# Kernel optimization log

Hardware: AMD Instinct MI355X
Metric: run time of the kernel (lower is better)

Reference implementation:

```python
import jax, jax.numpy as jnp
import numpy as np

EMBED = 192
EXPAND = 3
D1 = EMBED * EXPAND  # 576
RPE_IN = 32
LAYERS = 3
LAMBDA = 0.95


def _rpe_mlp(t, w0, b0, ws, bs, wo, bo):
    # t: (2n, 1) relative positions -> (2n, D1) Toeplitz coefficients
    h = t @ w0.T + b0
    for i in range(ws.shape[0]):
        h = jax.nn.relu(h) @ ws[i].T + bs[i]
    return jax.nn.relu(h) @ wo.T + bo


def _toeplitz(x, a):
    # Toeplitz matmul via length-2n circular convolution (FFT).
    # x: (B, n, d); a: (2n, d) coeffs ordered [t0, t1..t_{n-1}, pad, neg half]
    n = x.shape[1]
    m = 2 * n
    xf = jnp.fft.rfft(x, m, axis=1)
    af = jnp.fft.rfft(a, m, axis=0)
    return jnp.fft.irfft(xf * af[None], m, axis=1)[:, :n]


def _forward(x, p_w, p_b, q_w, q_b, v_w, v_b, o_w, o_b, slope,
             t1_w0, t1_b0, t1_ws, t1_bs, t1_wo, t1_bo,
             t2_w0, t2_b0, t2_ws, t2_bs, t2_wo, t2_bo):
    b, h, w, d = x.shape
    n = h  # square grid: h == w, rpe/decay built from n = x.shape[1]
    dt = x.dtype

    pos = jnp.arange(1, n, dtype=dt).reshape(-1, 1)          # (n-1, 1)
    zero = jnp.zeros((1, 1), dt)
    rpe_input = jnp.concatenate([zero, pos, zero, -pos], axis=0)  # (2n, 1)

    p = jax.nn.silu(x @ p_w.T + p_b)
    q = jax.nn.silu(x @ q_w.T + q_b)
    v = jax.nn.silu(x @ v_w.T + v_b)

    # decay mask: slope clamped to [0,1], blended with lambda, powered by |lag|
    sl = LAMBDA + (1.0 - LAMBDA) * jnp.clip(slope, 0.0, 1.0)  # (1, D1)
    idx = jnp.arange(1, n, dtype=dt).reshape(1, -1, 1)        # (1, n-1, 1)
    gamma = sl ** idx                                          # (1, n-1, D1)
    one = jnp.ones((1, 1, D1), dt)
    decay = jnp.concatenate([one, gamma, one, gamma[:, ::-1]], axis=1)[0]  # (2n, D1)

    a1 = _rpe_mlp(rpe_input, t1_w0, t1_b0, t1_ws, t1_bs, t1_wo, t1_bo) * decay
    a2 = _rpe_mlp(rpe_input, t2_w0, t2_b0, t2_ws, t2_bs, t2_wo, t2_bo) * decay

    qv = q * v                                                 # (b, h, w, D1)
    # axial mixing: tno1 along width, tno2 along height
    o1 = _toeplitz(qv.reshape(b * h, w, D1), a1).reshape(b, h, w, D1)
    o2 = _toeplitz(jnp.transpose(qv, (0, 2, 1, 3)).reshape(b * w, h, D1), a2)
    o2 = jnp.transpose(o2.reshape(b, w, h, D1), (0, 2, 1, 3))
    out = p * (o1 + o2)
    return out @ o_w.T + o_b


def setup_inputs() -> dict:
    key = jax.random.key(0)
    ks = jax.random.split(key, 8)

    def lin(k, out_d, in_d):
        k1, k2 = jax.random.split(k)
        s = 1.0 / np.sqrt(in_d)
        return (jax.random.uniform(k1, (out_d, in_d), jnp.float32, -s, s),
                jax.random.uniform(k2, (out_d,), jnp.float32, -s, s))

    x = jax.random.normal(ks[0], (8, 56, 56, EMBED), jnp.float32)
    p_w, p_b = lin(ks[1], D1, EMBED)
    q_w, q_b = lin(ks[2], D1, EMBED)
    v_w, v_b = lin(ks[3], D1, EMBED)
    o_w, o_b = lin(ks[4], EMBED, D1)
    # slope init: 1/arange(1, d1+1)^(1/(index+1)), index=0
    slope = (1.0 / jnp.arange(1, D1 + 1, dtype=jnp.float32)).reshape(1, -1)

    def tno_params(kb):
        kk = jax.random.split(kb, 2 + LAYERS)
        w0, b0 = lin(kk[0], RPE_IN, 1)
        ws, bs = [], []
        for i in range(LAYERS):
            wi, bi = lin(kk[1 + i], RPE_IN, RPE_IN)
            ws.append(wi); bs.append(bi)
        wo, bo = lin(kk[1 + LAYERS], D1, RPE_IN)
        return w0, b0, jnp.stack(ws), jnp.stack(bs), wo, bo

    t1 = tno_params(ks[5])
    t2 = tno_params(ks[6])
    return {"x": x, "p_w": p_w, "p_b": p_b, "q_w": q_w, "q_b": q_b,
            "v_w": v_w, "v_b": v_b, "o_w": o_w, "o_b": o_b, "slope": slope,
            "t1_w0": t1[0], "t1_b0": t1[1], "t1_ws": t1[2], "t1_bs": t1[3], "t1_wo": t1[4], "t1_bo": t1[5],
            "t2_w0": t2[0], "t2_b0": t2[1], "t2_ws": t2[2], "t2_bs": t2[3], "t2_wo": t2[4], "t2_bo": t2[5]}


def reference(x, p_w, p_b, q_w, q_b, v_w, v_b, o_w, o_b, slope,
              t1_w0, t1_b0, t1_ws, t1_bs, t1_wo, t1_bo,
              t2_w0, t2_b0, t2_ws, t2_bs, t2_wo, t2_bo):
    return _forward(x, p_w, p_b, q_w, q_b, v_w, v_b, o_w, o_b, slope,
                    t1_w0, t1_b0, t1_ws, t1_bs, t1_wo, t1_bo,
                    t2_w0, t2_b0, t2_ws, t2_bs, t2_wo, t2_bo)
```

## Files before the change

### kernel.cpp

```cpp
#include <hip/hip_runtime.h>
#include <hip/hip_bf16.h>
#include <math.h>

typedef unsigned short u16;
typedef short bf16x8 __attribute__((ext_vector_type(8)));
typedef float f32x4 __attribute__((ext_vector_type(4)));

#define NB 8
#define NN 56
#define M2 112
#define EMB 192
#define D1 576
#define TOK (NB*NN*NN)

__device__ __forceinline__ float bf2f(unsigned int u) {
    union { unsigned int i; float f; } v; v.i = u << 16; return v.f;
}
__device__ __forceinline__ u16 f2bf(float f) {
    union { float f; unsigned int i; } v; v.f = f;
    unsigned int x = v.i;
    return (u16)((x + 0x7fffu + ((x >> 16) & 1u)) >> 16);
}
__device__ __forceinline__ float silu(float x) {
    return x / (1.0f + __expf(-x));
}
__device__ __forceinline__ void async16(void* lds, const void* g) {
    __builtin_amdgcn_global_load_lds(
        (const __attribute__((address_space(1))) void*)g,
        (__attribute__((address_space(3))) void*)lds, 16, 0, 0);
}

#define XCH (TOK*EMB/4)
#define WCH (D1*EMB/4)
__global__ __launch_bounds__(256) void convert_kernel(
    const float* __restrict__ x,
    const float* __restrict__ pw, const float* __restrict__ qw,
    const float* __restrict__ vw, const float* __restrict__ ow,
    u16* __restrict__ xb, u16* __restrict__ wb, u16* __restrict__ owb)
{
    int tid = blockIdx.x * 256 + threadIdx.x;
    const float* src; u16* dst; int off;
    if (tid < XCH) { src = x; dst = xb; off = tid; }
    else {
        int r = tid - XCH;
        int seg = r / WCH; off = r % WCH;
        if (seg == 0)      { src = pw; dst = wb; }
        else if (seg == 1) { src = qw; dst = wb + D1*EMB; }
        else if (seg == 2) { src = vw; dst = wb + 2*D1*EMB; }
        else if (seg == 3) { src = ow; dst = owb; }
        else return;
    }
    float4 f = *(const float4*)(src + off * 4);
    ushort4 o;
    o.x = f2bf(f.x); o.y = f2bf(f.y); o.z = f2bf(f.z); o.w = f2bf(f.w);
    *(ushort4*)(dst + off * 4) = o;
}

__global__ __launch_bounds__(576) void rpe_kernel(
    const float* __restrict__ slope,
    const float* w0a, const float* b0a, const float* wsa, const float* bsa,
    const float* woa, const float* boa,
    const float* w0b, const float* b0b, const float* wsb, const float* bsb,
    const float* wob, const float* bob,
    float* __restrict__ A1, float* __restrict__ A2)
{
    int wq  = blockIdx.x / M2;
    int row = blockIdx.x % M2;
    const float* w0 = wq ? w0b : w0a;  const float* b0 = wq ? b0b : b0a;
    const float* ws = wq ? wsb : wsa;  const float* bs = wq ? bsb : bsa;
    const float* wo = wq ? wob : woa;  const float* bo = wq ? bob : boa;
    float* A = wq ? A2 : A1;

    float tval = (row == 0 || row == 56) ? 0.0f
               : (row < 56 ? (float)row : -(float)(row - 56));
    int kexp = (row == 0 || row == 56) ? 0 : (row < 56 ? row : 112 - row);

    __shared__ float h[32], g[32];
    int t = threadIdx.x;
    if (t < 32) h[t] = tval * w0[t] + b0[t];
    __syncthreads();
    for (int L = 0; L < 3; L++) {
        if (t < 32) g[t] = fmaxf(h[t], 0.0f);
        __syncthreads();
        float hn = 0.0f;
        if (t < 32) {
            hn = bs[L * 32 + t];
            for (int k = 0; k < 32; k++)
                hn = fmaf(g[k], ws[(L * 32 + t) * 32 + k], hn);
        }
        __syncthreads();
        if (t < 32) h[t] = hn;
        __syncthreads();
    }
    if (t < 32) g[t] = fmaxf(h[t], 0.0f);
    __syncthreads();

    float o = bo[t];
    for (int k = 0; k < 32; k++)
        o = fmaf(g[k], wo[t * 32 + k], o);

    float sl = slope[t];
    sl = 0.95f + 0.05f * fminf(fmaxf(sl, 0.0f), 1.0f);
    float dec = powf(sl, (float)kexp);
    A[row * D1 + t] = o * dec;
}

__global__ __launch_bounds__(256) void tbuild_kernel(
    const float* __restrict__ A1, const float* __restrict__ A2,
    u16* __restrict__ T1t, u16* __restrict__ T2t)
{
    int d = blockIdx.x;
    const float* src = blockIdx.y ? A2 : A1;
    u16* dst = blockIdx.y ? T2t : T1t;
    __shared__ float win[111];
    int t = threadIdx.x;
    if (t < 111) {
        int lag = t - 55;
        int rowi = lag + (lag < 0 ? 112 : 0);
        win[t] = src[rowi * D1 + d];
    }
    __syncthreads();
    int i = t >> 2, jq = (t & 3) * 16;
    u16 vals[16];
    #pragma unroll
    for (int jj = 0; jj < 16; jj++) {
        int j = jq + jj;
        float v = (i < 56 && j < 56) ? win[i - j + 55] : 0.0f;
        vals[jj] = f2bf(v);
    }
    u16* out = dst + ((size_t)d * 64 + i) * 64 + jq;
    *(uint4*)(out)     = *(uint4*)&vals[0];
    *(uint4*)(out + 8) = *(uint4*)&vals[8];
}

__global__ __launch_bounds__(256) void proj_kernel(
    const u16* __restrict__ xb, const u16* __restrict__ wb,
    const float* __restrict__ pb, const float* __restrict__ qb,
    const float* __restrict__ vb,
    u16* __restrict__ P_T, u16* __restrict__ QV_T)
{
    __shared__ u16 lds[40960];
    int m0 = blockIdx.x * 128, n0 = blockIdx.y * 64;
    int t = threadIdx.x;
    int l = t & 63, wave = t >> 6;
    int wm = wave >> 1, wn = wave & 1;
    int col16 = l & 15, q = l >> 4;

    f32x4 accp[4][2], accq[4][2], accv[4][2];
    #pragma unroll
    for (int i = 0; i < 4; i++)
        #pragma unroll
        for (int j = 0; j < 2; j++) {
            accp[i][j] = (f32x4){0,0,0,0};
            accq[i][j] = (f32x4){0,0,0,0};
            accv[i][j] = (f32x4){0,0,0,0};
        }

    auto stage = [&](int kc, int buf) {
        int bo = buf * 20480;
        #pragma unroll
        for (int ii = 0; ii < 4; ii++) {
            int slot = (ii * 4 + wave) * 64 + l;
            int r = slot >> 3, s = slot & 7;
            int g = s ^ (r & 7);
            async16(&lds[bo + slot * 8], xb + (m0 + r) * EMB + kc * 64 + g * 8);
        }
        #pragma unroll
        for (int ii = 0; ii < 6; ii++) {
            int slot = (ii * 4 + wave) * 64 + l;
            int mat = slot >> 9, cc = slot & 511;
            int r = cc >> 3, s = cc & 7;
            int g = s ^ (r & 7);
            async16(&lds[bo + 8192 + slot * 8],
                    wb + mat * (D1 * EMB) + (n0 + r) * EMB + kc * 64 + g * 8);
        }
    };

    stage(0, 0);
    __syncthreads();

    #pragma unroll
    for (int kc = 0; kc < 3; kc++) {
        int buf = kc & 1;
        if (kc < 2) stage(kc + 1, buf ^ 1);
        int bo = buf * 20480;
        #pragma unroll
        for (int kk = 0; kk < 2; kk++) {
            bf16x8 af[4];
            #pragma unroll
            for (int mt = 0; mt < 4; mt++) {
                int row = wm * 64 + mt * 16 + col16;
                int sw = (q + 4 * kk) ^ (col16 & 7);
                af[mt] = *(const bf16x8*)&lds[bo + row * 64 + sw * 8];
            }
            bf16x8 bfr[3][2];
            #pragma unroll
            for (int mat = 0; mat < 3; mat++)
                #pragma unroll
                for (int nt = 0; nt < 2; nt++) {
                    int row = wn * 32 + nt * 16 + col16;
                    int sw = (q + 4 * kk) ^ (col16 & 7);
                    bfr[mat][nt] = *(const bf16x8*)&lds[bo + 8192 + mat * 4096 + row * 64 + sw * 8];
                }
            #pragma unroll
            for (int mt = 0; mt < 4; mt++)
                #pragma unroll
                for (int nt = 0; nt < 2; nt++) {
                    accp[mt][nt] = __builtin_amdgcn_mfma_f32_16x16x32_bf16(
                        af[mt], bfr[0][nt], accp[mt][nt], 0, 0, 0);
                    accq[mt][nt] = __builtin_amdgcn_mfma_f32_16x16x32_bf16(
                        af[mt], bfr[1][nt], accq[mt][nt], 0, 0, 0);
                    accv[mt][nt] = __builtin_amdgcn_mfma_f32_16x16x32_bf16(
                        af[mt], bfr[2][nt], accv[mt][nt], 0, 0, 0);
                }
        }
        __syncthreads();
    }

    u16* scr = lds + wave * 2688;
    float pbv[2], qbv[2], vbv[2];
    #pragma unroll
    for (int nt = 0; nt < 2; nt++) {
        int n = n0 + wn * 32 + nt * 16 + col16;
        pbv[nt] = pb[n]; qbv[nt] = qb[n]; vbv[nt] = vb[n];
    }
    int tok = (l & 31) * 2;
    int dh = l >> 5;
    #pragma unroll
    for (int mt = 0; mt < 4; mt++)
        #pragma unroll
        for (int nt = 0; nt < 2; nt++)
            #pragma unroll
            for (int r = 0; r < 4; r++)
                scr[(mt * 16 + q * 4 + r) * 42 + nt * 16 + col16] =
                    f2bf(silu(accp[mt][nt][r] + pbv[nt]));
    #pragma unroll
    for (int i = 0; i < 16; i++) {
        int dl = i * 2 + dh;
        unsigned int v = (unsigned int)scr[tok * 42 + dl] |
                         ((unsigned int)scr[(tok + 1) * 42 + dl] << 16);
        *(unsigned int*)&P_T[(size_t)(n0 + wn * 32 + dl) * TOK + m0 + wm * 64 + tok] = v;
    }
    #pragma unroll
    for (int mt = 0; mt < 4; mt++)
        #pragma unroll
        for (int nt = 0; nt < 2; nt++)
            #pragma unroll
            for (int r = 0; r < 4; r++)
                scr[(mt * 16 + q * 4 + r) * 42 + nt * 16 + col16] =
                    f2bf(silu(accq[mt][nt][r] + qbv[nt]) *
                         silu(accv[mt][nt][r] + vbv[nt]));
    #pragma unroll
    for (int i = 0; i < 16; i++) {
        int dl = i * 2 + dh;
        unsigned int v = (unsigned int)scr[tok * 42 + dl] |
                         ((unsigned int)scr[(tok + 1) * 42 + dl] << 16);
        *(unsigned int*)&QV_T[(size_t)(n0 + wn * 32 + dl) * TOK + m0 + wm * 64 + tok] = v;
    }
}

__global__ __launch_bounds__(256) void tno_mfma(
    const u16* __restrict__ QV_T, const u16* __restrict__ T1t,
    const u16* __restrict__ T2t, const u16* __restrict__ P_T,
    u16* __restrict__ U_T)
{
    __shared__ u16 T1s[4096];
    __shared__ u16 T2s[4096];
    __shared__ u16 Qn[64 * 72];
    __shared__ u16 Qt[64 * 72];
    __shared__ float O1f[56 * 68];
    int d = blockIdx.x, b = blockIdx.y;
    int t = threadIdx.x;
    size_t base = (size_t)d * TOK + (size_t)b * 3136;

    #pragma unroll
    for (int k = 0; k < 2; k++) {
        int slot = t + k * 256;
        int i = slot >> 3, s = slot & 7;
        int g = s ^ (i & 7);
        async16(&T1s[slot * 8], T1t + ((size_t)d * 64 + i) * 64 + g * 8);
        async16(&T2s[slot * 8], T2t + ((size_t)d * 64 + i) * 64 + g * 8);
    }
    for (int c = t; c < 392; c += 256) {
        int h = c / 7, w8 = (c % 7) * 8;
        uint4 v = *(const uint4*)(QV_T + base + c * 8);
        *(uint4*)&Qn[h * 72 + w8] = v;
        u16 e[8];
        *(uint4*)e = v;
        #pragma unroll
        for (int k = 0; k < 8; k++)
            Qt[(w8 + k) * 72 + h] = e[k];
    }
    if (t < 56) {
        uint4 z = {0, 0, 0, 0};
        *(uint4*)&Qn[t * 72 + 56] = z;
        *(uint4*)&Qt[t * 72 + 56] = z;
    }
    __syncthreads();

    int l = t & 63, wave = t >> 6;
    int col16 = l & 15, q = l >> 4;

    f32x4 acc1[4], acc2[4];
    #pragma unroll
    for (int i = 0; i < 4; i++) { acc1[i] = (f32x4){0,0,0,0}; acc2[i] = (f32x4){0,0,0,0}; }

    #pragma unroll
    for (int kk = 0; kk < 2; kk++) {
        int sw = ((q + 4 * kk) ^ (col16 & 7)) * 8;
        bf16x8 bq1 = *(const bf16x8*)&Qn[(wave * 16 + col16) * 72 + kk * 32 + q * 8];
        bf16x8 bq2 = *(const bf16x8*)&Qt[(wave * 16 + col16) * 72 + kk * 32 + q * 8];
        #pragma unroll
        for (int mt = 0; mt < 4; mt++) {
            bf16x8 a1 = *(const bf16x8*)&T1s[(mt * 16 + col16) * 64 + sw];
            bf16x8 a2 = *(const bf16x8*)&T2s[(mt * 16 + col16) * 64 + sw];
            acc1[mt] = __builtin_amdgcn_mfma_f32_16x16x32_bf16(a1, bq1, acc1[mt], 0, 0, 0);
            acc2[mt] = __builtin_amdgcn_mfma_f32_16x16x32_bf16(a2, bq2, acc2[mt], 0, 0, 0);
        }
    }

    {
        int n = wave * 16 + col16;
        if (n < 56) {
            #pragma unroll
            for (int mt = 0; mt < 4; mt++)
                #pragma unroll
                for (int r = 0; r < 4; r++) {
                    int m = mt * 16 + q * 4 + r;
                    if (m < 56) O1f[n * 68 + m] = acc1[mt][r];
                }
        }
    }
    __syncthreads();
    {
        int n = wave * 16 + col16;
        if (n < 56) {
            #pragma unroll
            for (int mt = 0; mt < 4; mt++)
                #pragma unroll
                for (int r = 0; r < 4; r++) {
                    int m = mt * 16 + q * 4 + r;
                    if (m < 56) O1f[m * 68 + n] += acc2[mt][r];
                }
        }
    }
    __syncthreads();
    for (int c = t; c < 392; c += 256) {
        int h = c / 7, w8 = (c % 7) * 8;
        f32x4 s0 = *(const f32x4*)&O1f[h * 68 + w8];
        f32x4 s1 = *(const f32x4*)&O1f[h * 68 + w8 + 4];
        uint4 pv = *(const uint4*)(P_T + base + c * 8);
        u16 pe[8];
        *(uint4*)pe = pv;
        u16 ue[8];
        #pragma unroll
        for (int k = 0; k < 4; k++) ue[k] = f2bf(bf2f(pe[k]) * s0[k]);
        #pragma unroll
        for (int k = 0; k < 4; k++) ue[4 + k] = f2bf(bf2f(pe[4 + k]) * s1[k]);
        *(uint4*)(U_T + base + c * 8) = *(uint4*)ue;
    }
}

__global__ __launch_bounds__(256) void transp_kernel(
    const u16* __restrict__ U_T, u16* __restrict__ U)
{
    __shared__ u16 tile[64 * 72];
    int t = threadIdx.x;
    int t0 = blockIdx.x * 64;
    int d0 = blockIdx.y * 64;
    {
        int dr = t >> 2, c = t & 3;
        #pragma unroll
        for (int h = 0; h < 2; h++) {
            int cc = c + h * 4;
            uint4 v = *(const uint4*)(U_T + (size_t)(d0 + dr) * TOK + t0 + cc * 8);
            *(uint4*)&tile[dr * 72 + cc * 8] = v;
        }
    }
    __syncthreads();
    {
        int tr = t & 63, c4 = t >> 6;
        u16 vals[16];
        #pragma unroll
        for (int k = 0; k < 16; k++)
            vals[k] = tile[(c4 * 16 + k) * 72 + tr];
        u16* dst = U + (size_t)(t0 + tr) * D1 + d0 + c4 * 16;
        *(uint4*)(dst)     = *(uint4*)&vals[0];
        *(uint4*)(dst + 8) = *(uint4*)&vals[8];
    }
}

__global__ __launch_bounds__(256) void outproj_kernel(
    const u16* __restrict__ U, const u16* __restrict__ owb,
    const float* __restrict__ ob, float* __restrict__ out)
{
    __shared__ char ldsraw[36864];
    u16* As = (u16*)ldsraw;
    u16* Bs = (u16*)(ldsraw + 16384);
    int m0 = blockIdx.x * 128, n0 = blockIdx.y * 64;
    int t = threadIdx.x;
    int l = t & 63, wave = t >> 6;
    int wm = wave >> 1, wn = wave & 1;
    int col16 = l & 15, q = l >> 4;

    f32x4 acc[4][2];
    #pragma unroll
    for (int i = 0; i < 4; i++)
        #pragma unroll
        for (int j = 0; j < 2; j++) acc[i][j] = (f32x4){0,0,0,0};

    for (int k0 = 0; k0 < D1; k0 += 64) {
        #pragma unroll
        for (int ii = 0; ii < 4; ii++) {
            int slot = (ii * 4 + wave) * 64 + l;
            int r = slot >> 3, s = slot & 7;
            int g = s ^ (r & 7);
            async16(&As[slot * 8], U + (m0 + r) * D1 + k0 + g * 8);
        }
        #pragma unroll
        for (int ii = 0; ii < 2; ii++) {
            int slot = (ii * 4 + wave) * 64 + l;
            int r = slot >> 3, s = slot & 7;
            int g = s ^ (r & 7);
            async16(&Bs[slot * 8], owb + (n0 + r) * D1 + k0 + g * 8);
        }
        __syncthreads();

        #pragma unroll
        for (int kk = 0; kk < 2; kk++) {
            int sw = (q + 4 * kk) ^ (col16 & 7);
            bf16x8 af[4];
            #pragma unroll
            for (int mt = 0; mt < 4; mt++)
                af[mt] = *(const bf16x8*)&As[(wm * 64 + mt * 16 + col16) * 64 + sw * 8];
            bf16x8 bfr[2];
            #pragma unroll
            for (int nt = 0; nt < 2; nt++)
                bfr[nt] = *(const bf16x8*)&Bs[(wn * 32 + nt * 16 + col16) * 64 + sw * 8];
            #pragma unroll
            for (int mt = 0; mt < 4; mt++)
                #pragma unroll
                for (int nt = 0; nt < 2; nt++)
                    acc[mt][nt] = __builtin_amdgcn_mfma_f32_16x16x32_bf16(
                        af[mt], bfr[nt], acc[mt][nt], 0, 0, 0);
        }
        __syncthreads();
    }

    float* scr = (float*)ldsraw + wave * 2304;
    float obv[2];
    #pragma unroll
    for (int nt = 0; nt < 2; nt++)
        obv[nt] = ob[n0 + wn * 32 + nt * 16 + col16];
    #pragma unroll
    for (int mt = 0; mt < 4; mt++)
        #pragma unroll
        for (int nt = 0; nt < 2; nt++)
            #pragma unroll
            for (int r = 0; r < 4; r++)
                scr[(mt * 16 + q * 4 + r) * 36 + nt * 16 + col16] =
                    acc[mt][nt][r] + obv[nt];
    #pragma unroll
    for (int k = 0; k < 8; k++) {
        int row = k * 8 + (l >> 3), cs = (l & 7) * 4;
        f32x4 v = *(const f32x4*)&scr[row * 36 + cs];
        *(f32x4*)&out[(m0 + wm * 64 + row) * EMB + n0 + wn * 32 + cs] = v;
    }
}

extern "C" void kernel_launch(void* const* d_in, const int* in_sizes, int n_in,
                              void* d_out, int out_size, void* d_ws, size_t ws_size,
                              hipStream_t stream)
{
    (void)in_sizes; (void)n_in; (void)out_size; (void)ws_size;
    const float* x     = (const float*)d_in[0];
    const float* p_w   = (const float*)d_in[1];
    const float* p_b   = (const float*)d_in[2];
    const float* q_w   = (const float*)d_in[3];
    const float* q_b   = (const float*)d_in[4];
    const float* v_w   = (const float*)d_in[5];
    const float* v_b   = (const float*)d_in[6];
    const float* o_w   = (const float*)d_in[7];
    const float* o_b   = (const float*)d_in[8];
    const float* slope = (const float*)d_in[9];
    const float* t1_w0 = (const float*)d_in[10];
    const float* t1_b0 = (const float*)d_in[11];
    const float* t1_ws = (const float*)d_in[12];
    const float* t1_bs = (const float*)d_in[13];
    const float* t1_wo = (const float*)d_in[14];
    const float* t1_bo = (const float*)d_in[15];
    const float* t2_w0 = (const float*)d_in[16];
    const float* t2_b0 = (const float*)d_in[17];
    const float* t2_ws = (const float*)d_in[18];
    const float* t2_bs = (const float*)d_in[19];
    const float* t2_wo = (const float*)d_in[20];
    const float* t2_bo = (const float*)d_in[21];

    char* ws = (char*)d_ws;
    float* A1  = (float*)ws;
    float* A2  = (float*)(ws + 258048);
    u16*   PU  = (u16*)(ws + 516096);
    u16*   QVT = (u16*)(ws + 29417472);
    u16*   UT  = (u16*)(ws + 58318848);
    u16*   xb  = (u16*)(ws + 87220224);
    u16*   wb  = (u16*)(ws + 96854016);
    u16*   owb = (u16*)(ws + 97517568);
    u16*   T1t = (u16*)(ws + 97738752);
    u16*   T2t = (u16*)(ws + 102457344);

    convert_kernel<<<(XCH + 4*WCH + 255) / 256, 256, 0, stream>>>(
        x, p_w, q_w, v_w, o_w, xb, wb, owb);
    rpe_kernel<<<224, 576, 0, stream>>>(slope,
        t1_w0, t1_b0, t1_ws, t1_bs, t1_wo, t1_bo,
        t2_w0, t2_b0, t2_ws, t2_bs, t2_wo, t2_bo, A1, A2);
    tbuild_kernel<<<dim3(576, 2), 256, 0, stream>>>(A1, A2, T1t, T2t);
    proj_kernel<<<dim3(TOK / 128, D1 / 64), 256, 0, stream>>>(
        xb, wb, p_b, q_b, v_b, PU, QVT);
    tno_mfma<<<dim3(D1, NB), 256, 0, stream>>>(QVT, T1t, T2t, PU, UT);
    transp_kernel<<<dim3(TOK / 64, D1 / 64), 256, 0, stream>>>(UT, PU);
    outproj_kernel<<<dim3(TOK / 128, EMB / 64), 256, 0, stream>>>(
        PU, owb, o_b, (float*)d_out);
}
```

Baseline: 224.1 us.

## Fuse transpose into outproj, widen proj to 512 threads with direct stores

Removes the standalone transpose kernel: outproj now loads the channel-major U_T tile into LDS and transposes it there before the MFMA loop. proj_kernel moves to 512 threads with 16-column wave tiles and a three-stage vmcnt-based pipeline. It also stores P_T/QV_T directly as ushort4 instead of staging through LDS, and uses an exp2/rcp silu. This saves a full global round trip of the intermediate tensor and one launch. The cost is an extra LDS transpose in outproj and narrower, less coalesced stores in proj.

```diff
diff --git a/kernel.cpp b/kernel.cpp
--- a/kernel.cpp
+++ b/kernel.cpp
@@ -21,8 +21,9 @@
     unsigned int x = v.i;
     return (u16)((x + 0x7fffu + ((x >> 16) & 1u)) >> 16);
 }
-__device__ __forceinline__ float silu(float x) {
-    return x / (1.0f + __expf(-x));
+__device__ __forceinline__ float fast_silu(float x) {
+    float e = __builtin_amdgcn_exp2f(-1.442695041f * x);
+    return x * __builtin_amdgcn_rcpf(1.0f + e);
 }
 __device__ __forceinline__ void async16(void* lds, const void* g) {
     __builtin_amdgcn_global_load_lds(
@@ -133,7 +134,7 @@
     *(uint4*)(out + 8) = *(uint4*)&vals[8];
 }
 
-__global__ __launch_bounds__(256) void proj_kernel(
+__global__ __launch_bounds__(512, 4) void proj_kernel(
     const u16* __restrict__ xb, const u16* __restrict__ wb,
     const float* __restrict__ pb, const float* __restrict__ qb,
     const float* __restrict__ vb,
@@ -143,31 +144,29 @@
     int m0 = blockIdx.x * 128, n0 = blockIdx.y * 64;
     int t = threadIdx.x;
     int l = t & 63, wave = t >> 6;
-    int wm = wave >> 1, wn = wave & 1;
+    int wm = wave >> 2, wn = wave & 3;
     int col16 = l & 15, q = l >> 4;
 
-    f32x4 accp[4][2], accq[4][2], accv[4][2];
-    #pragma unroll
-    for (int i = 0; i < 4; i++)
-        #pragma unroll
-        for (int j = 0; j < 2; j++) {
-            accp[i][j] = (f32x4){0,0,0,0};
-            accq[i][j] = (f32x4){0,0,0,0};
-            accv[i][j] = (f32x4){0,0,0,0};
-        }
+    f32x4 accp[4], accq[4], accv[4];
+    #pragma unroll
+    for (int i = 0; i < 4; i++) {
+        accp[i] = (f32x4){0,0,0,0};
+        accq[i] = (f32x4){0,0,0,0};
+        accv[i] = (f32x4){0,0,0,0};
+    }
 
     auto stage = [&](int kc, int buf) {
         int bo = buf * 20480;
         #pragma unroll
-        for (int ii = 0; ii < 4; ii++) {
-            int slot = (ii * 4 + wave) * 64 + l;
+        for (int ii = 0; ii < 2; ii++) {
+            int slot = ii * 512 + t;
             int r = slot >> 3, s = slot & 7;
             int g = s ^ (r & 7);
             async16(&lds[bo + slot * 8], xb + (m0 + r) * EMB + kc * 64 + g * 8);
         }
         #pragma unroll
-        for (int ii = 0; ii < 6; ii++) {
-            int slot = (ii * 4 + wave) * 64 + l;
+        for (int ii = 0; ii < 3; ii++) {
+            int slot = ii * 512 + t;
             int mat = slot >> 9, cc = slot & 511;
             int r = cc >> 3, s = cc & 7;
             int g = s ^ (r & 7);
@@ -176,86 +175,61 @@
         }
     };
 
+    auto compute = [&](int bo) {
+        #pragma unroll
+        for (int kk = 0; kk < 2; kk++) {
+            int sw = ((q + 4 * kk) ^ (col16 & 7)) * 8;
+            bf16x8 af[4];
+            #pragma unroll
+            for (int mt = 0; mt < 4; mt++)
+                af[mt] = *(const bf16x8*)&lds[bo + (wm * 64 + mt * 16 + col16) * 64 + sw];
+            bf16x8 bfr[3];
+            #pragma unroll
+            for (int mat = 0; mat < 3; mat++)
+                bfr[mat] = *(const bf16x8*)&lds[bo + 8192 + mat * 4096 + (wn * 16 + col16) * 64 + sw];
+            #pragma unroll
+            for (int mt = 0; mt < 4; mt++) {
+                accp[mt] = __builtin_amdgcn_mfma_f32_16x16x32_bf16(af[mt], bfr[0], accp[mt], 0, 0, 0);
+                accq[mt] = __builtin_amdgcn_mfma_f32_16x16x32_bf16(af[mt], bfr[1], accq[mt], 0, 0, 0);
+                accv[mt] = __builtin_amdgcn_mfma_f32_16x16x32_bf16(af[mt], bfr[2], accv[mt], 0, 0, 0);
+            }
+        }
+    };
+
     stage(0, 0);
-    __syncthreads();
-
-    #pragma unroll
-    for (int kc = 0; kc < 3; kc++) {
-        int buf = kc & 1;
-        if (kc < 2) stage(kc + 1, buf ^ 1);
-        int bo = buf * 20480;
-        #pragma unroll
-        for (int kk = 0; kk < 2; kk++) {
-            bf16x8 af[4];
-            #pragma unroll
-            for (int mt = 0; mt < 4; mt++) {
-                int row = wm * 64 + mt * 16 + col16;
-                int sw = (q + 4 * kk) ^ (col16 & 7);
-                af[mt] = *(const bf16x8*)&lds[bo + row * 64 + sw * 8];
-            }
-            bf16x8 bfr[3][2];
-            #pragma unroll
-            for (int mat = 0; mat < 3; mat++)
-                #pragma unroll
-                for (int nt = 0; nt < 2; nt++) {
-                    int row = wn * 32 + nt * 16 + col16;
-                    int sw = (q + 4 * kk) ^ (col16 & 7);
-                    bfr[mat][nt] = *(const bf16x8*)&lds[bo + 8192 + mat * 4096 + row * 64 + sw * 8];
-                }
-            #pragma unroll
-            for (int mt = 0; mt < 4; mt++)
-                #pragma unroll
-                for (int nt = 0; nt < 2; nt++) {
-                    accp[mt][nt] = __builtin_amdgcn_mfma_f32_16x16x32_bf16(
-                        af[mt], bfr[0][nt], accp[mt][nt], 0, 0, 0);
-                    accq[mt][nt] = __builtin_amdgcn_mfma_f32_16x16x32_bf16(
-                        af[mt], bfr[1][nt], accq[mt][nt], 0, 0, 0);
-                    accv[mt][nt] = __builtin_amdgcn_mfma_f32_16x16x32_bf16(
-                        af[mt], bfr[2][nt], accv[mt][nt], 0, 0, 0);
-                }
-        }
-        __syncthreads();
-    }
-
-    u16* scr = lds + wave * 2688;
-    float pbv[2], qbv[2], vbv[2];
-    #pragma unroll
-    for (int nt = 0; nt < 2; nt++) {
-        int n = n0 + wn * 32 + nt * 16 + col16;
-        pbv[nt] = pb[n]; qbv[nt] = qb[n]; vbv[nt] = vb[n];
-    }
-    int tok = (l & 31) * 2;
-    int dh = l >> 5;
-    #pragma unroll
-    for (int mt = 0; mt < 4; mt++)
-        #pragma unroll
-        for (int nt = 0; nt < 2; nt++)
-            #pragma unroll
-            for (int r = 0; r < 4; r++)
-                scr[(mt * 16 + q * 4 + r) * 42 + nt * 16 + col16] =
-                    f2bf(silu(accp[mt][nt][r] + pbv[nt]));
-    #pragma unroll
-    for (int i = 0; i < 16; i++) {
-        int dl = i * 2 + dh;
-        unsigned int v = (unsigned int)scr[tok * 42 + dl] |
-                         ((unsigned int)scr[(tok + 1) * 42 + dl] << 16);
-        *(unsigned int*)&P_T[(size_t)(n0 + wn * 32 + dl) * TOK + m0 + wm * 64 + tok] = v;
-    }
-    #pragma unroll
-    for (int mt = 0; mt < 4; mt++)
-        #pragma unroll
-        for (int nt = 0; nt < 2; nt++)
-            #pragma unroll
-            for (int r = 0; r < 4; r++)
-                scr[(mt * 16 + q * 4 + r) * 42 + nt * 16 + col16] =
-                    f2bf(silu(accq[mt][nt][r] + qbv[nt]) *
-                         silu(accv[mt][nt][r] + vbv[nt]));
-    #pragma unroll
-    for (int i = 0; i < 16; i++) {
-        int dl = i * 2 + dh;
-        unsigned int v = (unsigned int)scr[tok * 42 + dl] |
-                         ((unsigned int)scr[(tok + 1) * 42 + dl] << 16);
-        *(unsigned int*)&QV_T[(size_t)(n0 + wn * 32 + dl) * TOK + m0 + wm * 64 + tok] = v;
+    stage(1, 1);
+    asm volatile("s_waitcnt vmcnt(5)" ::: "memory");
+    __builtin_amdgcn_s_barrier();
+    compute(0);
+    __builtin_amdgcn_s_barrier();
+    stage(2, 0);
+    asm volatile("s_waitcnt vmcnt(5)" ::: "memory");
+    __builtin_amdgcn_s_barrier();
+    compute(20480);
+    asm volatile("s_waitcnt vmcnt(0)" ::: "memory");
+    __builtin_amdgcn_s_barrier();
+    compute(0);
+
+    int n = n0 + wn * 16 + col16;
+    float pbv = pb[n], qbv = qb[n], vbv = vb[n];
+    size_t drow = (size_t)n * TOK + m0 + wm * 64;
+    #pragma unroll
+    for (int mt = 0; mt < 4; mt++) {
+        ushort4 o;
+        o.x = f2bf(fast_silu(accp[mt][0] + pbv));
+        o.y = f2bf(fast_silu(accp[mt][1] + pbv));
+        o.z = f2bf(fast_silu(accp[mt][2] + pbv));
+        o.w = f2bf(fast_silu(accp[mt][3] + pbv));
+        *(ushort4*)&P_T[drow + mt * 16 + q * 4] = o;
+    }
+    #pragma unroll
+    for (int mt = 0; mt < 4; mt++) {
+        ushort4 o;
+        o.x = f2bf(fast_silu(accq[mt][0] + qbv) * fast_silu(accv[mt][0] + vbv));
+        o.y = f2bf(fast_silu(accq[mt][1] + qbv) * fast_silu(accv[mt][1] + vbv));
+        o.z = f2bf(fast_silu(accq[mt][2] + qbv) * fast_silu(accv[mt][2] + vbv));
+        o.w = f2bf(fast_silu(accq[mt][3] + qbv) * fast_silu(accv[mt][3] + vbv));
+        *(ushort4*)&QV_T[drow + mt * 16 + q * 4] = o;
     }
 }
 
@@ -361,42 +335,14 @@
     }
 }
 
-__global__ __launch_bounds__(256) void transp_kernel(
-    const u16* __restrict__ U_T, u16* __restrict__ U)
-{
-    __shared__ u16 tile[64 * 72];
-    int t = threadIdx.x;
-    int t0 = blockIdx.x * 64;
-    int d0 = blockIdx.y * 64;
-    {
-        int dr = t >> 2, c = t & 3;
-        #pragma unroll
-        for (int h = 0; h < 2; h++) {
-            int cc = c + h * 4;
-            uint4 v = *(const uint4*)(U_T + (size_t)(d0 + dr) * TOK + t0 + cc * 8);
-            *(uint4*)&tile[dr * 72 + cc * 8] = v;
-        }
-    }
-    __syncthreads();
-    {
-        int tr = t & 63, c4 = t >> 6;
-        u16 vals[16];
-        #pragma unroll
-        for (int k = 0; k < 16; k++)
-            vals[k] = tile[(c4 * 16 + k) * 72 + tr];
-        u16* dst = U + (size_t)(t0 + tr) * D1 + d0 + c4 * 16;
-        *(uint4*)(dst)     = *(uint4*)&vals[0];
-        *(uint4*)(dst + 8) = *(uint4*)&vals[8];
-    }
-}
-
 __global__ __launch_bounds__(256) void outproj_kernel(
-    const u16* __restrict__ U, const u16* __restrict__ owb,
+    const u16* __restrict__ U_T, const u16* __restrict__ owb,
     const float* __restrict__ ob, float* __restrict__ out)
 {
-    __shared__ char ldsraw[36864];
-    u16* As = (u16*)ldsraw;
-    u16* Bs = (u16*)(ldsraw + 16384);
+    __shared__ char ldsraw[40960];
+    u16* Uscr = (u16*)ldsraw;
+    u16* As   = (u16*)(ldsraw + 16384);
+    u16* Bs   = (u16*)(ldsraw + 32768);
     int m0 = blockIdx.x * 128, n0 = blockIdx.y * 64;
     int t = threadIdx.x;
     int l = t & 63, wave = t >> 6;
@@ -409,34 +355,47 @@
         #pragma unroll
         for (int j = 0; j < 2; j++) acc[i][j] = (f32x4){0,0,0,0};
 
-    for (int k0 = 0; k0 < D1; k0 += 64) {
+    for (int k0 = 0; k0 < 9; k0++) {
         #pragma unroll
         for (int ii = 0; ii < 4; ii++) {
-            int slot = (ii * 4 + wave) * 64 + l;
+            int slot = ii * 256 + t;
+            int dd = slot >> 4, tk = slot & 15;
+            async16(&Uscr[slot * 8],
+                    U_T + (size_t)(k0 * 64 + dd) * TOK + m0 + tk * 8);
+        }
+        #pragma unroll
+        for (int ii = 0; ii < 2; ii++) {
+            int slot = ii * 256 + t;
             int r = slot >> 3, s = slot & 7;
             int g = s ^ (r & 7);
-            async16(&As[slot * 8], U + (m0 + r) * D1 + k0 + g * 8);
-        }
-        #pragma unroll
-        for (int ii = 0; ii < 2; ii++) {
-            int slot = (ii * 4 + wave) * 64 + l;
-            int r = slot >> 3, s = slot & 7;
-            int g = s ^ (r & 7);
-            async16(&Bs[slot * 8], owb + (n0 + r) * D1 + k0 + g * 8);
+            async16(&Bs[slot * 8], owb + (n0 + r) * D1 + k0 * 64 + g * 8);
+        }
+        asm volatile("s_waitcnt vmcnt(2)" ::: "memory");
+        __builtin_amdgcn_s_barrier();
+        #pragma unroll
+        for (int ii = 0; ii < 4; ii++) {
+            int c = ii * 256 + t;
+            int tok = c & 127, dc = c >> 7;
+            u16 e[8];
+            #pragma unroll
+            for (int j = 0; j < 8; j++)
+                e[j] = Uscr[(dc * 8 + j) * 128 + tok];
+            int s = dc ^ (tok & 7);
+            *(uint4*)&As[tok * 64 + s * 8] = *(uint4*)e;
         }
         __syncthreads();
 
         #pragma unroll
         for (int kk = 0; kk < 2; kk++) {
-            int sw = (q + 4 * kk) ^ (col16 & 7);
+            int sw = ((q + 4 * kk) ^ (col16 & 7)) * 8;
             bf16x8 af[4];
             #pragma unroll
             for (int mt = 0; mt < 4; mt++)
-                af[mt] = *(const bf16x8*)&As[(wm * 64 + mt * 16 + col16) * 64 + sw * 8];
+                af[mt] = *(const bf16x8*)&As[(wm * 64 + mt * 16 + col16) * 64 + sw];
             bf16x8 bfr[2];
             #pragma unroll
             for (int nt = 0; nt < 2; nt++)
-                bfr[nt] = *(const bf16x8*)&Bs[(wn * 32 + nt * 16 + col16) * 64 + sw * 8];
+                bfr[nt] = *(const bf16x8*)&Bs[(wn * 32 + nt * 16 + col16) * 64 + sw];
             #pragma unroll
             for (int mt = 0; mt < 4; mt++)
                 #pragma unroll
@@ -460,6 +419,7 @@
             for (int r = 0; r < 4; r++)
                 scr[(mt * 16 + q * 4 + r) * 36 + nt * 16 + col16] =
                     acc[mt][nt][r] + obv[nt];
+    __syncthreads();
     #pragma unroll
     for (int k = 0; k < 8; k++) {
         int row = k * 8 + (l >> 3), cs = (l & 7) * 4;
@@ -499,7 +459,7 @@
     char* ws = (char*)d_ws;
     float* A1  = (float*)ws;
     float* A2  = (float*)(ws + 258048);
-    u16*   PU  = (u16*)(ws + 516096);
+    u16*   PT  = (u16*)(ws + 516096);
     u16*   QVT = (u16*)(ws + 29417472);
     u16*   UT  = (u16*)(ws + 58318848);
     u16*   xb  = (u16*)(ws + 87220224);
@@ -514,10 +474,9 @@
         t1_w0, t1_b0, t1_ws, t1_bs, t1_wo, t1_bo,
         t2_w0, t2_b0, t2_ws, t2_bs, t2_wo, t2_bo, A1, A2);
     tbuild_kernel<<<dim3(576, 2), 256, 0, stream>>>(A1, A2, T1t, T2t);
-    proj_kernel<<<dim3(TOK / 128, D1 / 64), 256, 0, stream>>>(
-        xb, wb, p_b, q_b, v_b, PU, QVT);
-    tno_mfma<<<dim3(D1, NB), 256, 0, stream>>>(QVT, T1t, T2t, PU, UT);
-    transp_kernel<<<dim3(TOK / 64, D1 / 64), 256, 0, stream>>>(UT, PU);
+    proj_kernel<<<dim3(TOK / 128, D1 / 64), 512, 0, stream>>>(
+        xb, wb, p_b, q_b, v_b, PT, QVT);
+    tno_mfma<<<dim3(D1, NB), 256, 0, stream>>>(QVT, T1t, T2t, PT, UT);
     outproj_kernel<<<dim3(TOK / 128, EMB / 64), 256, 0, stream>>>(
-        PU, owb, o_b, (float*)d_out);
-}
+        UT, owb, o_b, (float*)d_out);
+}
```

New measurement: 200.8 us. 10.4% less time.
